# Optimization experiments

Hardware: AMD Instinct MI355X
Metric: run time of the kernel (lower is better)

The kernel has to match this reference:

```python
import jax, jax.numpy as jnp
import numpy as np

B, T, E, NH, VOCAB, MULT = 1, 1024, 768, 12, 32000, 32
N = E * MULT // NH  # 2048
LN_EPS = 1e-5


def setup_inputs() -> dict:
    key = jax.random.key(0)
    ks = jax.random.split(key, 6)
    return {
        "idx": jax.random.randint(ks[0], (B, T), 0, VOCAB),
        "embed": jax.random.normal(ks[1], (VOCAB, E), jnp.float32) * 0.02,
        "encoder": jax.random.normal(ks[2], (NH, E, N), jnp.float32) * 0.02,
        "encoder_v": jax.random.normal(ks[3], (NH, E, N), jnp.float32) * 0.02,
        "decoder": jax.random.normal(ks[4], (NH * N, E), jnp.float32) * 0.02,
        "lm_head": jax.random.normal(ks[5], (VOCAB, E), jnp.float32) * 0.02,
        "ln_w": jnp.ones((E,), jnp.float32),
        "ln_b": jnp.zeros((E,), jnp.float32),
        "n_layer": 6,
    }


def reference(idx, embed, encoder, encoder_v, decoder, lm_head, ln_w, ln_b, n_layer):
    nh, e, n = encoder.shape
    t = idx.shape[1]
    dec = decoder.reshape(nh, n, e)  # flatten order (h, n) -> h*N + n

    def ln(x):
        m = jnp.mean(x, axis=-1, keepdims=True)
        v = jnp.mean(jnp.square(x - m), axis=-1, keepdims=True)
        return (x - m) * jax.lax.rsqrt(v + LN_EPS) * ln_w + ln_b

    causal = jnp.tril(jnp.ones((t, t), bool))  # [T, T]
    scale = 1.0 / np.sqrt(n).astype(np.float32)

    x = ln(embed[idx])  # [B, T, E]  (the unsqueezed head dim broadcasts; keep it squeezed)
    for _ in range(n_layer):
        # encoder projection + ReLU: [B,T,E] x [H,E,N] -> [B,H,T,N]
        x_sparse = jax.nn.relu(jnp.einsum("bte,hen->bhtn", x, encoder))
        # hand-rolled causal attention, Q=K=x_sparse, V=x (broadcast over heads)
        scores = jnp.einsum("bhqn,bhkn->bhqk", x_sparse, x_sparse) * scale
        scores = jnp.where(causal, scores, -jnp.inf)
        attn = jax.nn.softmax(scores, axis=-1)
        y = jnp.einsum("bhqk,bke->bhqe", attn, x)  # [B,H,T,E]
        y = ln(y)
        y_sparse = jax.nn.relu(jnp.einsum("bhte,hen->bhtn", y, encoder_v))
        xy = x_sparse * y_sparse  # [B,H,T,N]; dropout p=0 -> identity
        y_mlp = jnp.einsum("bhtn,hne->bte", xy, dec)  # decoder matmul
        x = ln(x + ln(y_mlp))
    logits = jnp.einsum("bte,ve->btv", x, lm_head)
    return logits
```

## Files before the change

kernel.cpp:

```cpp
#include <hip/hip_runtime.h>

typedef unsigned short u16;
typedef short bf16x8 __attribute__((ext_vector_type(8)));
typedef float f32x4 __attribute__((ext_vector_type(4)));
typedef u16 u16x4 __attribute__((ext_vector_type(4)));

#define TT     1024
#define EE     768
#define NHH    12
#define ND     2048
#define VOC    32000
#define HNN    24576
#define NLAYER 6
#define LN_EPS 1e-5f
#define SPLITK 16

__device__ __forceinline__ float b2f(u16 u){
  unsigned int x = ((unsigned int)u) << 16; float f; __builtin_memcpy(&f, &x, 4); return f;
}
__device__ __forceinline__ u16 f2b(float f){
  unsigned int x; __builtin_memcpy(&x, &f, 4);
  x = x + 0x7fffu + ((x >> 16) & 1u);
  return (u16)(x >> 16);
}

__device__ __forceinline__ void gload16(const void* g, void* lds){
  __builtin_amdgcn_global_load_lds(
      (const __attribute__((address_space(1))) unsigned int*)g,
      (__attribute__((address_space(3))) unsigned int*)(unsigned int)(unsigned long long)lds,
      16, 0, 0);
}

__device__ __forceinline__ bf16x8 ldsr(unsigned addr){
  bf16x8 r;
  asm volatile("ds_read_b128 %0, %1" : "=v"(r) : "v"(addr));
  return r;
}

__device__ __forceinline__ void blk_sum2(float& a, float& b){
  #pragma unroll
  for (int o = 32; o > 0; o >>= 1){ a += __shfl_down(a, o); b += __shfl_down(b, o); }
  __shared__ float sa[4], sb[4];
  int lane = threadIdx.x & 63, wid = threadIdx.x >> 6;
  __syncthreads();
  if (lane == 0){ sa[wid] = a; sb[wid] = b; }
  __syncthreads();
  a = (sa[0] + sa[1]) + (sa[2] + sa[3]);
  b = (sb[0] + sb[1]) + (sb[2] + sb[3]);
}
__device__ __forceinline__ float blk_max(float v){
  #pragma unroll
  for (int o = 32; o > 0; o >>= 1) v = fmaxf(v, __shfl_down(v, o));
  __shared__ float sm[4];
  int lane = threadIdx.x & 63, wid = threadIdx.x >> 6;
  __syncthreads();
  if (lane == 0) sm[wid] = v;
  __syncthreads();
  return fmaxf(fmaxf(sm[0], sm[1]), fmaxf(sm[2], sm[3]));
}
__device__ __forceinline__ float blk_sum(float v){
  #pragma unroll
  for (int o = 32; o > 0; o >>= 1) v += __shfl_down(v, o);
  __shared__ float ss[4];
  int lane = threadIdx.x & 63, wid = threadIdx.x >> 6;
  __syncthreads();
  if (lane == 0) ss[wid] = v;
  __syncthreads();
  return (ss[0] + ss[1]) + (ss[2] + ss[3]);
}

__global__ void transpose_f2b(const float* __restrict__ in, long sIn,
                              u16* __restrict__ out, long sOut, int R, int Cc){
  __shared__ float tile[32][33];
  int z = blockIdx.z;
  in  += (long)z * sIn;
  out += (long)z * sOut;
  int c0 = blockIdx.x * 32, r0 = blockIdx.y * 32;
  int lx = threadIdx.x & 31, ly = threadIdx.x >> 5;
  #pragma unroll
  for (int i = 0; i < 32; i += 8)
    tile[ly + i][lx] = in[(long)(r0 + ly + i) * Cc + (c0 + lx)];
  __syncthreads();
  #pragma unroll
  for (int i = 0; i < 32; i += 8)
    out[(long)(c0 + ly + i) * R + (r0 + lx)] = f2b(tile[lx][ly + i]);
}

__global__ void conv_f2b(const float* __restrict__ in, u16* __restrict__ out){
  long i = ((long)blockIdx.x * 256 + threadIdx.x) * 4;
  float4 v = *(const float4*)(in + i);
  u16x4 o; o.x = f2b(v.x); o.y = f2b(v.y); o.z = f2b(v.z); o.w = f2b(v.w);
  *(u16x4*)(out + i) = o;
}

__global__ void xpose(const u16* __restrict__ in, u16* __restrict__ out){
  __shared__ u16 t[64][65];
  int e0 = blockIdx.x * 64, t0 = blockIdx.y * 64;
  int lx = threadIdx.x & 63, ly = threadIdx.x >> 6;
  #pragma unroll
  for (int i = 0; i < 64; i += 4)
    t[ly + i][lx] = in[(long)(t0 + ly + i) * EE + e0 + lx];
  __syncthreads();
  #pragma unroll
  for (int i = 0; i < 64; i += 4)
    out[(long)(e0 + ly + i) * TT + t0 + lx] = t[lx][ly + i];
}

__global__ void embed_ln(const int* __restrict__ idx, const float* __restrict__ emb,
                         const float* __restrict__ w, const float* __restrict__ b,
                         float* __restrict__ xf, u16* __restrict__ xb){
  int t = blockIdx.x, tid = threadIdx.x;
  const float* src = emb + (long)idx[t] * EE;
  float v[3];
  #pragma unroll
  for (int j = 0; j < 3; j++) v[j] = src[tid + j * 256];
  float s = v[0] + v[1] + v[2];
  float s2 = v[0]*v[0] + v[1]*v[1] + v[2]*v[2];
  blk_sum2(s, s2);
  float m  = s * (1.0f / EE);
  float var = s2 * (1.0f / EE) - m * m;
  float rs = rsqrtf(var + LN_EPS);
  #pragma unroll
  for (int j = 0; j < 3; j++){
    int e = tid + j * 256;
    float o = (v[j] - m) * rs * w[e] + b[e];
    xf[(long)t * EE + e] = o;
    xb[(long)t * EE + e] = f2b(o);
  }
}

__global__ void ln_rows(const u16* __restrict__ in, u16* __restrict__ out,
                        const float* __restrict__ w, const float* __restrict__ b){
  long row = blockIdx.x; int tid = threadIdx.x;
  const u16* src = in + row * EE;
  float v[3];
  #pragma unroll
  for (int j = 0; j < 3; j++) v[j] = b2f(src[tid + j * 256]);
  float s = v[0] + v[1] + v[2];
  float s2 = v[0]*v[0] + v[1]*v[1] + v[2]*v[2];
  blk_sum2(s, s2);
  float m = s * (1.0f / EE);
  float var = s2 * (1.0f / EE) - m * m;
  float rs = rsqrtf(var + LN_EPS);
  #pragma unroll
  for (int j = 0; j < 3; j++){
    int e = tid + j * 256;
    out[row * EE + e] = f2b((v[j] - m) * rs * w[e] + b[e]);
  }
}

__global__ void softmax_rows(const u16* __restrict__ scores, u16* __restrict__ attn){
  int q = blockIdx.x, h = blockIdx.y, tid = threadIdx.x;
  const u16* srow = scores + ((long)h * TT + q) * TT;
  u16* arow = attn + ((long)h * TT + q) * TT;
  const int len = q + 1;
  const int pad = (q + 128) & ~127;
  float v[4];
  float mx = -1e30f;
  #pragma unroll
  for (int j = 0; j < 4; j++){
    int i = tid + j * 256;
    if (i < len){ v[j] = b2f(srow[i]); mx = fmaxf(mx, v[j]); }
  }
  mx = blk_max(mx);
  float s = 0.f;
  #pragma unroll
  for (int j = 0; j < 4; j++){
    int i = tid + j * 256;
    if (i < len){ v[j] = __expf(v[j] - mx); s += v[j]; }
  }
  float inv = 1.0f / blk_sum(s);
  #pragma unroll
  for (int j = 0; j < 4; j++){
    int i = tid + j * 256;
    if (i < pad){
      u16 o = 0;
      if (i < len) o = f2b(v[j] * inv);
      arow[i] = o;
    }
  }
}

template<int P>
__global__ void residual_ln(const u16* __restrict__ part, const float* __restrict__ xin,
                            float* __restrict__ xf, u16* __restrict__ xb,
                            const float* __restrict__ w, const float* __restrict__ b){
  int t = blockIdx.x, tid = threadIdx.x;
  float g[3];
  #pragma unroll
  for (int j = 0; j < 3; j++){
    int e = tid + j * 256;
    float s = 0.f;
    #pragma unroll
    for (int pp = 0; pp < P; pp++) s += b2f(part[((long)pp * TT + t) * EE + e]);
    g[j] = s;
  }
  float s = g[0] + g[1] + g[2], s2 = g[0]*g[0] + g[1]*g[1] + g[2]*g[2];
  blk_sum2(s, s2);
  float m = s * (1.0f / EE), var = s2 * (1.0f / EE) - m * m;
  float rs = rsqrtf(var + LN_EPS);
  float hh[3];
  #pragma unroll
  for (int j = 0; j < 3; j++){
    int e = tid + j * 256;
    hh[j] = xin[(long)t * EE + e] + ((g[j] - m) * rs * w[e] + b[e]);
  }
  s = hh[0] + hh[1] + hh[2]; s2 = hh[0]*hh[0] + hh[1]*hh[1] + hh[2]*hh[2];
  blk_sum2(s, s2);
  m = s * (1.0f / EE); var = s2 * (1.0f / EE) - m * m; rs = rsqrtf(var + LN_EPS);
  #pragma unroll
  for (int j = 0; j < 3; j++){
    int e = tid + j * 256;
    float o = (hh[j] - m) * rs * w[e] + b[e];
    xf[(long)t * EE + e] = o;
    xb[(long)t * EE + e] = f2b(o);
  }
}

template<int EPI>
__global__ __launch_bounds__(512, 2)
void g8(const u16* __restrict__ Ab, long sA,
        const u16* __restrict__ Bb, long sB,
        void* __restrict__ Cb, long sC,
        int grid_m, int grid_mn,
        int K, int lda, int ldb, int ldc, float scale,
        const u16* __restrict__ Mul, long sMul, int ldmul){
  __shared__ __align__(16) u16 S[69632];

  const int nwg = gridDim.x, orig = blockIdx.x;
  const int q = nwg >> 3, r = nwg & 7, xcd = orig & 7;
  const int wgid = (xcd < r ? xcd*(q+1) : r*(q+1) + (xcd - r)*q) + (orig >> 3);
  const int z   = wgid / grid_mn;
  const int rem = wgid - z*grid_mn;
  const int nb  = rem / grid_m;
  const int mb  = rem - nb*grid_m;
  const int m0 = mb*256, n0 = nb*256;
  const int tid = threadIdx.x, lane = tid & 63, wid = tid >> 6;

  if (EPI == 2 && n0 > m0 + 255) return;

  const u16* A = Ab + (long)z*sA;
  const u16* B = Bb + (long)z*sB;

  const int rS = wid*16 + (lane >> 2);
  const int cS = (((lane & 3) ^ ((rS >> 1) & 3)) << 3);
  const u16* gA = A + (long)(m0 + rS)*lda + cS;
  const u16* gB = B + (long)(n0 + rS)*ldb + cS;

  char* Sb = (char*)&S[0];
  const unsigned db0 = 0, db1 = 65536u, scr = 131072u;
  auto issue = [&](const u16* src, unsigned dstOff){
    gload16(src, Sb + dstOff + (unsigned)wid*1024u);
  };

  const int wr = wid >> 2, wc = wid & 3;
  const int fr = lane & 15, fk = lane >> 4;
  const unsigned base = (unsigned)(unsigned long long)Sb;
  unsigned aOff[8], bOff[4];
  #pragma unroll
  for (int mi = 0; mi < 8; mi++){
    int row = wr*128 + mi*16 + fr;
    aOff[mi] = (unsigned)(row*64 + ((fk ^ ((row >> 1) & 3)) << 4));
  }
  #pragma unroll
  for (int ni = 0; ni < 4; ni++){
    int row = wc*64 + ni*16 + fr;
    bOff[ni] = 32768u + (unsigned)(row*64 + ((fk ^ ((row >> 1) & 3)) << 4));
  }

  const int NT = K >> 6;
  const long lda128 = (long)128*lda, ldb128 = (long)128*ldb;

  f32x4 acc[8][4] = {};

  issue(gA,              db0);          issue(gA + lda128,          db0 + 8192u);
  issue(gB,              db0+32768u);   issue(gB + ldb128,          db0 + 40960u);
  issue(gA + 32,         db0+16384u);   issue(gA + 32 + lda128,     db0 + 24576u);
  issue(gB + 32,         db0+49152u);   issue(gB + 32 + ldb128,     db0 + 57344u);
  issue(gA + 64,         db1);          issue(gA + 64 + lda128,     db1 + 8192u);
  issue(gB + 64,         db1+32768u);   issue(gB + 64 + ldb128,     db1 + 40960u);
  asm volatile("s_waitcnt vmcnt(8)" ::: "memory");
  __builtin_amdgcn_s_barrier();
  __builtin_amdgcn_sched_barrier(0);

  for (int t = 0; t < NT; t++){
    const unsigned cur = (t & 1) ? db1 : db0;
    const unsigned oth = (t & 1) ? db0 : db1;
    const bool v1 = (t + 1 < NT), v2 = (t + 2 < NT);
    const long k1 = (long)(v1 ? t + 1 : 0) * 64;
    const long k2 = (long)(v2 ? t + 2 : 0) * 64;
    const unsigned d1A = v1 ? oth + 16384u : scr;
    const unsigned d1B = v1 ? oth + 49152u : scr;
    const unsigned d2A = v2 ? cur           : scr;
    const unsigned d2B = v2 ? cur + 32768u  : scr;
    bf16x8 a[4], b[4];

    #pragma unroll
    for (int ni = 0; ni < 4; ni++) b[ni] = ldsr(base + cur + bOff[ni]);
    #pragma unroll
    for (int u = 0; u < 4; u++)    a[u]  = ldsr(base + cur + aOff[u]);
    issue(gA + k1 + 32, d1A); issue(gA + k1 + 32 + lda128, d1A + 8192u);
    __builtin_amdgcn_s_barrier();
    asm volatile("s_waitcnt lgkmcnt(0)" ::: "memory");
    __builtin_amdgcn_sched_barrier(0);
    __builtin_amdgcn_s_setprio(1);
    #pragma unroll
    for (int u = 0; u < 4; u++)
      #pragma unroll
      for (int ni = 0; ni < 4; ni++)
        acc[u][ni] = __builtin_amdgcn_mfma_f32_16x16x32_bf16(a[u], b[ni], acc[u][ni], 0, 0, 0);
    __builtin_amdgcn_s_setprio(0);
    __builtin_amdgcn_s_barrier();
    __builtin_amdgcn_sched_barrier(0);

    #pragma unroll
    for (int u = 0; u < 4; u++) a[u] = ldsr(base + cur + aOff[4 + u]);
    issue(gB + k1 + 32, d1B); issue(gB + k1 + 32 + ldb128, d1B + 8192u);
    __builtin_amdgcn_s_barrier();
    asm volatile("s_waitcnt lgkmcnt(0)" ::: "memory");
    __builtin_amdgcn_sched_barrier(0);
    __builtin_amdgcn_s_setprio(1);
    #pragma unroll
    for (int u = 0; u < 4; u++)
      #pragma unroll
      for (int ni = 0; ni < 4; ni++)
        acc[4+u][ni] = __builtin_amdgcn_mfma_f32_16x16x32_bf16(a[u], b[ni], acc[4+u][ni], 0, 0, 0);
    __builtin_amdgcn_s_setprio(0);
    asm volatile("s_waitcnt vmcnt(8)" ::: "memory");
    __builtin_amdgcn_s_barrier();
    __builtin_amdgcn_sched_barrier(0);

    #pragma unroll
    for (int ni = 0; ni < 4; ni++) b[ni] = ldsr(base + cur + bOff[ni] + 16384u);
    #pragma unroll
    for (int u = 0; u < 4; u++)    a[u]  = ldsr(base + cur + aOff[u] + 16384u);
    issue(gA + k2, d2A); issue(gA + k2 + lda128, d2A + 8192u);
    __builtin_amdgcn_s_barrier();
    asm volatile("s_waitcnt lgkmcnt(0)" ::: "memory");
    __builtin_amdgcn_sched_barrier(0);
    __builtin_amdgcn_s_setprio(1);
    #pragma unroll
    for (int u = 0; u < 4; u++)
      #pragma unroll
      for (int ni = 0; ni < 4; ni++)
        acc[u][ni] = __builtin_amdgcn_mfma_f32_16x16x32_bf16(a[u], b[ni], acc[u][ni], 0, 0, 0);
    __builtin_amdgcn_s_setprio(0);
    __builtin_amdgcn_s_barrier();
    __builtin_amdgcn_sched_barrier(0);

    #pragma unroll
    for (int u = 0; u < 4; u++) a[u] = ldsr(base + cur + aOff[4 + u] + 16384u);
    issue(gB + k2, d2B); issue(gB + k2 + ldb128, d2B + 8192u);
    __builtin_amdgcn_s_barrier();
    asm volatile("s_waitcnt lgkmcnt(0)" ::: "memory");
    __builtin_amdgcn_sched_barrier(0);
    __builtin_amdgcn_s_setprio(1);
    #pragma unroll
    for (int u = 0; u < 4; u++)
      #pragma unroll
      for (int ni = 0; ni < 4; ni++)
        acc[4+u][ni] = __builtin_amdgcn_mfma_f32_16x16x32_bf16(a[u], b[ni], acc[4+u][ni], 0, 0, 0);
    __builtin_amdgcn_s_setprio(0);
    asm volatile("s_waitcnt vmcnt(8)" ::: "memory");
    __builtin_amdgcn_s_barrier();
    __builtin_amdgcn_sched_barrier(0);
  }
  asm volatile("s_waitcnt vmcnt(0)" ::: "memory");

  const int er = (lane >> 4) * 4, ec = lane & 15;
  #pragma unroll
  for (int mi = 0; mi < 8; mi++){
    #pragma unroll
    for (int ni = 0; ni < 4; ni++){
      #pragma unroll
      for (int j = 0; j < 4; j++){
        int row = m0 + wr*128 + mi*16 + er + j;
        int col = n0 + wc*64 + ni*16 + ec;
        float v = acc[mi][ni][j];
        if (EPI == 0){
          ((float*)Cb + (long)z * sC)[(long)row * ldc + col] = v;
        } else if (EPI == 1){
          v = v > 0.f ? v : 0.f;
          ((u16*)Cb + (long)z * sC)[(long)row * ldc + col] = f2b(v);
        } else if (EPI == 2){
          ((u16*)Cb + (long)z * sC)[(long)row * ldc + col] = f2b(v * scale);
        } else {
          v = v > 0.f ? v : 0.f;
          float mfv = b2f((Mul + (long)z * sMul)[(long)row * ldmul + col]);
          ((u16*)Cb + (long)z * sC)[(long)row * ldc + col] = f2b(v * mfv);
        }
      }
    }
  }
}

template<int EPI, bool CCLAMP>
__global__ __launch_bounds__(256, 2)
void gemmw(const u16* __restrict__ Ab, long sA,
           const u16* __restrict__ Bb, long sB,
           void* __restrict__ Cb, long sC,
           int grid_m, int grid_mn,
           int K, int lda, int ldb, int ldc){
  constexpr unsigned BUFB = 24576u;
  __shared__ __align__(16) u16 S[3 * 12288];

  const int nwg = gridDim.x, orig = blockIdx.x;
  const int q = nwg >> 3, r = nwg & 7, xcd = orig & 7;
  const int wgid = (xcd < r ? xcd*(q+1) : r*(q+1) + (xcd - r)*q) + (orig >> 3);
  const int z   = wgid / grid_mn;
  const int rem = wgid - z*grid_mn;
  const int nb  = rem / grid_m;
  const int mb  = rem - nb*grid_m;
  const int m0 = mb*128, n0 = nb*256;
  const int tid = threadIdx.x, lane = tid & 63, wid = tid >> 6;

  const u16* A = Ab + (long)z*sA;
  const u16* B = Bb + (long)z*sB;

  const int rS = tid >> 2;
  const int cS = (((tid & 3) ^ ((rS >> 1) & 3)) << 3);
  const u16* gA[2]; const u16* gB[4];
  #pragma unroll
  for (int i = 0; i < 2; i++) gA[i] = A + (long)(m0 + i*64 + rS)*lda + cS;
  #pragma unroll
  for (int i = 0; i < 4; i++) gB[i] = B + (long)(n0 + i*64 + rS)*ldb + cS;

  char* Sb = (char*)&S[0];
  auto stage = [&](int kt, unsigned bB){
    const int ko = kt << 5;
    gload16(gA[0] + ko, Sb + bB +          wid*1024u);
    gload16(gA[1] + ko, Sb + bB +  4096u + wid*1024u);
    #pragma unroll
    for (int i = 0; i < 4; i++)
      gload16(gB[i] + ko, Sb + bB + 8192u + i*4096u + wid*1024u);
  };

  const int wr = wid >> 1, wc = wid & 1;
  const int fr = lane & 15, fk = lane >> 4;
  const unsigned base = (unsigned)(unsigned long long)Sb;
  unsigned aAd[4], bAd[8];
  #pragma unroll
  for (int mi = 0; mi < 4; mi++){
    int row = wr*64 + mi*16 + fr;
    aAd[mi] = base + (unsigned)(row*64 + ((fk ^ ((row >> 1) & 3)) << 4));
  }
  #pragma unroll
  for (int ni = 0; ni < 8; ni++){
    int row = wc*128 + ni*16 + fr;
    bAd[ni] = base + 8192u + (unsigned)(row*64 + ((fk ^ ((row >> 1) & 3)) << 4));
  }

  const int Keff = CCLAMP ? (m0 + 128 < K ? m0 + 128 : K) : K;
  const int NT = Keff >> 5;
  const int s0 = (mb*13 + nb*7 + z*5) % NT;

  f32x4 acc[4][8] = {};

  int p1 = s0 + 1; if (p1 >= NT) p1 -= NT;
  stage(s0, 0);
  stage(p1, BUFB);
  asm volatile("s_waitcnt vmcnt(6)" ::: "memory");
  __builtin_amdgcn_s_barrier();
  __builtin_amdgcn_sched_barrier(0);

  unsigned rbB = 0, wbB = 2u*BUFB;
  for (int t = 0; t < NT; t++){
    int nx = (t + 2 < NT) ? t + 2 : NT - 1;
    int ph = s0 + nx; if (ph >= NT) ph -= NT;
    stage(ph, wbB);
    bf16x8 afr[4], bfr[8];
    #pragma unroll
    for (int ni = 0; ni < 8; ni++) bfr[ni] = ldsr(bAd[ni] + rbB);
    #pragma unroll
    for (int mi = 0; mi < 4; mi++) afr[mi] = ldsr(aAd[mi] + rbB);
    __builtin_amdgcn_s_barrier();
    asm volatile("s_waitcnt lgkmcnt(0)" ::: "memory");
    __builtin_amdgcn_sched_barrier(0);
    __builtin_amdgcn_s_setprio(1);
    #pragma unroll
    for (int mi = 0; mi < 4; mi++)
      #pragma unroll
      for (int ni = 0; ni < 8; ni++)
        acc[mi][ni] = __builtin_amdgcn_mfma_f32_16x16x32_bf16(afr[mi], bfr[ni], acc[mi][ni], 0, 0, 0);
    __builtin_amdgcn_s_setprio(0);
    __builtin_amdgcn_sched_barrier(0);
    asm volatile("s_waitcnt vmcnt(6)" ::: "memory");
    __builtin_amdgcn_s_barrier();
    __builtin_amdgcn_sched_barrier(0);
    unsigned tmp = rbB; rbB += BUFB; if (rbB == 3u*BUFB) rbB = 0;
    wbB = tmp;
  }
  asm volatile("s_waitcnt vmcnt(0)" ::: "memory");

  const int er = (lane >> 4) * 4, ec = lane & 15;
  #pragma unroll
  for (int mi = 0; mi < 4; mi++){
    #pragma unroll
    for (int ni = 0; ni < 8; ni++){
      #pragma unroll
      for (int j = 0; j < 4; j++){
        int row = m0 + wr*64 + mi*16 + er + j;
        int col = n0 + wc*128 + ni*16 + ec;
        float v = acc[mi][ni][j];
        if (EPI == 0){
          ((float*)Cb + (long)z * sC)[(long)row * ldc + col] = v;
        } else {
          ((u16*)Cb + (long)z * sC)[(long)row * ldc + col] = f2b(v);
        }
      }
    }
  }
}

extern "C" void kernel_launch(void* const* d_in, const int* in_sizes, int n_in,
                              void* d_out, int out_size, void* d_ws, size_t ws_size,
                              hipStream_t stream){
  (void)in_sizes; (void)n_in; (void)out_size; (void)ws_size;
  const int*   idx     = (const int*)  d_in[0];
  const float* embed   = (const float*)d_in[1];
  const float* encoder = (const float*)d_in[2];
  const float* encv    = (const float*)d_in[3];
  const float* decoder = (const float*)d_in[4];
  const float* lm_head = (const float*)d_in[5];
  const float* ln_w    = (const float*)d_in[6];
  const float* ln_b    = (const float*)d_in[7];
  float* out = (float*)d_out;

  char* p = (char*)d_ws;
  auto take = [&](size_t n){ char* r = p; p += (n + 255) & ~(size_t)255; return r; };
  u16*   encT  = (u16*)  take((size_t)NHH * ND * EE * 2);
  u16*   encvT = (u16*)  take((size_t)NHH * ND * EE * 2);
  u16*   decT  = (u16*)  take((size_t)EE * HNN * 2);
  u16*   lmhB  = (u16*)  take((size_t)VOC * EE * 2);
  float* xf    = (float*)take((size_t)TT * EE * 4);
  u16*   xb    = (u16*)  take((size_t)TT * EE * 2);
  u16*   xT    = (u16*)  take((size_t)EE * TT * 2);
  u16*   xs    = (u16*)  take((size_t)NHH * TT * ND * 2);
  char*  big   =         take((size_t)NHH * TT * TT * 4);
  u16*   attn  = (u16*)  take((size_t)NHH * TT * TT * 2);
  u16*   yb    = (u16*)  take((size_t)NHH * TT * EE * 2);
  take((size_t)8 * TT * EE * 4);
  u16*   scores = (u16*)big;
  u16*   ybig   = (u16*)big;
  u16*   xy     = (u16*)big;
  u16*   part   = attn;

  dim3 blk(256, 1, 1);

  transpose_f2b<<<dim3(ND / 32, EE / 32, NHH), blk, 0, stream>>>(encoder, (long)EE * ND, encT,  (long)ND * EE, EE, ND);
  transpose_f2b<<<dim3(ND / 32, EE / 32, NHH), blk, 0, stream>>>(encv,    (long)EE * ND, encvT, (long)ND * EE, EE, ND);
  transpose_f2b<<<dim3(EE / 32, HNN / 32, 1),  blk, 0, stream>>>(decoder, 0, decT, 0, HNN, EE);
  conv_f2b<<<dim3((VOC * EE) / 1024, 1, 1), blk, 0, stream>>>(lm_head, lmhB);

  embed_ln<<<dim3(TT, 1, 1), blk, 0, stream>>>(idx, embed, ln_w, ln_b, xf, xb);
  xpose<<<dim3(EE / 64, TT / 64, 1), blk, 0, stream>>>(xb, xT);

  const float scl = 0.022097086912079608f;

  for (int L = 0; L < NLAYER; ++L){
    g8<1><<<dim3(4*8*NHH), dim3(512), 0, stream>>>(
        xb, 0, encT, (long)ND * EE, xs, (long)TT * ND,
        4, 32, EE, EE, EE, ND, 0.f, (const u16*)0, 0, 0);
    g8<2><<<dim3(4*4*NHH), dim3(512), 0, stream>>>(
        xs, (long)TT * ND, xs, (long)TT * ND, scores, (long)TT * TT,
        4, 16, ND, ND, ND, TT, scl, (const u16*)0, 0, 0);
    softmax_rows<<<dim3(TT, NHH, 1), blk, 0, stream>>>(scores, attn);
    gemmw<4,true><<<dim3(8*3*NHH), blk, 0, stream>>>(
        attn, (long)TT * TT, xT, 0, ybig, (long)TT * EE,
        8, 24, TT, TT, TT, EE);
    ln_rows<<<dim3(NHH * TT, 1, 1), blk, 0, stream>>>(ybig, yb, ln_w, ln_b);
    g8<3><<<dim3(4*8*NHH), dim3(512), 0, stream>>>(
        yb, (long)TT * EE, encvT, (long)ND * EE, xy, (long)ND,
        4, 32, EE, EE, EE, HNN, 0.f, xs, (long)TT * ND, ND);
    gemmw<4,false><<<dim3(8*3*SPLITK), blk, 0, stream>>>(
        xy, (long)(HNN / SPLITK), decT, (long)(HNN / SPLITK), part, (long)TT * EE,
        8, 24, HNN / SPLITK, HNN, HNN, EE);
    residual_ln<SPLITK><<<dim3(TT, 1, 1), blk, 0, stream>>>(part, xf, xf, xb, ln_w, ln_b);
    xpose<<<dim3(EE / 64, TT / 64, 1), blk, 0, stream>>>(xb, xT);
  }

  g8<0><<<dim3(4*125), dim3(512), 0, stream>>>(
      xb, 0, lmhB, 0, out, 0,
      4, 500, EE, EE, EE, VOC, 0.f, (const u16*)0, 0, 0);
}
```

Before: 1.927 ms.

## Fuse weight prep kernels, vectorize row kernels, rotate GEMM K start

Merges the four weight transpose and convert launches into one prep kernel. The layernorm, softmax and residual row kernels move to 4-wide vector loads and stores with 192 active threads. The g8 GEMM now starts its K loop at a per-tile rotated offset and wraps around, which removes the scratch LDS region for out-of-range prefetches and shrinks shared memory. The rotation is meant to spread concurrent tiles across different K slices of memory, at the cost of a changed summation order.

```diff
diff --git a/kernel.cpp b/kernel.cpp
--- a/kernel.cpp
+++ b/kernel.cpp
@@ -69,28 +69,44 @@
   return (ss[0] + ss[1]) + (ss[2] + ss[3]);
 }
 
-__global__ void transpose_f2b(const float* __restrict__ in, long sIn,
-                              u16* __restrict__ out, long sOut, int R, int Cc){
+__global__ void prep(const float* __restrict__ enc, const float* __restrict__ encv,
+                     const float* __restrict__ dec, const float* __restrict__ lmh,
+                     u16* __restrict__ encT, u16* __restrict__ encvT,
+                     u16* __restrict__ decT, u16* __restrict__ lmhB){
   __shared__ float tile[32][33];
-  int z = blockIdx.z;
-  in  += (long)z * sIn;
-  out += (long)z * sOut;
-  int c0 = blockIdx.x * 32, r0 = blockIdx.y * 32;
+  int b = blockIdx.x;
   int lx = threadIdx.x & 31, ly = threadIdx.x >> 5;
-  #pragma unroll
-  for (int i = 0; i < 32; i += 8)
-    tile[ly + i][lx] = in[(long)(r0 + ly + i) * Cc + (c0 + lx)];
-  __syncthreads();
-  #pragma unroll
-  for (int i = 0; i < 32; i += 8)
-    out[(long)(c0 + ly + i) * R + (r0 + lx)] = f2b(tile[lx][ly + i]);
-}
-
-__global__ void conv_f2b(const float* __restrict__ in, u16* __restrict__ out){
-  long i = ((long)blockIdx.x * 256 + threadIdx.x) * 4;
-  float4 v = *(const float4*)(in + i);
-  u16x4 o; o.x = f2b(v.x); o.y = f2b(v.y); o.z = f2b(v.z); o.w = f2b(v.w);
-  *(u16x4*)(out + i) = o;
+  if (b < 36864){
+    const float* in; u16* out;
+    if (b < 18432){ in = enc; out = encT; } else { in = encv; out = encvT; b -= 18432; }
+    int z = b / 1536, rem = b - z * 1536;
+    int c0 = (rem & 63) * 32, r0 = (rem >> 6) * 32;
+    in  += (long)z * EE * ND;
+    out += (long)z * ND * EE;
+    #pragma unroll
+    for (int i = 0; i < 32; i += 8)
+      tile[ly + i][lx] = in[(long)(r0 + ly + i) * ND + c0 + lx];
+    __syncthreads();
+    #pragma unroll
+    for (int i = 0; i < 32; i += 8)
+      out[(long)(c0 + ly + i) * EE + r0 + lx] = f2b(tile[lx][ly + i]);
+  } else if (b < 55296){
+    b -= 36864;
+    int c0 = (b % 24) * 32, r0 = (b / 24) * 32;
+    #pragma unroll
+    for (int i = 0; i < 32; i += 8)
+      tile[ly + i][lx] = dec[(long)(r0 + ly + i) * EE + c0 + lx];
+    __syncthreads();
+    #pragma unroll
+    for (int i = 0; i < 32; i += 8)
+      decT[(long)(c0 + ly + i) * HNN + r0 + lx] = f2b(tile[lx][ly + i]);
+  } else {
+    b -= 55296;
+    long i = ((long)b * 256 + threadIdx.x) * 4;
+    float4 v = *(const float4*)(lmh + i);
+    u16x4 o; o.x = f2b(v.x); o.y = f2b(v.y); o.z = f2b(v.z); o.w = f2b(v.w);
+    *(u16x4*)(lmhB + i) = o;
+  }
 }
 
 __global__ void xpose(const u16* __restrict__ in, u16* __restrict__ out){
@@ -111,21 +127,28 @@
                          float* __restrict__ xf, u16* __restrict__ xb){
   int t = blockIdx.x, tid = threadIdx.x;
   const float* src = emb + (long)idx[t] * EE;
-  float v[3];
-  #pragma unroll
-  for (int j = 0; j < 3; j++) v[j] = src[tid + j * 256];
-  float s = v[0] + v[1] + v[2];
-  float s2 = v[0]*v[0] + v[1]*v[1] + v[2]*v[2];
+  float v[4] = {0.f, 0.f, 0.f, 0.f};
+  if (tid < 192){
+    float4 r = *(const float4*)&src[tid * 4];
+    v[0] = r.x; v[1] = r.y; v[2] = r.z; v[3] = r.w;
+  }
+  float s = (v[0] + v[1]) + (v[2] + v[3]);
+  float s2 = (v[0]*v[0] + v[1]*v[1]) + (v[2]*v[2] + v[3]*v[3]);
   blk_sum2(s, s2);
   float m  = s * (1.0f / EE);
   float var = s2 * (1.0f / EE) - m * m;
   float rs = rsqrtf(var + LN_EPS);
-  #pragma unroll
-  for (int j = 0; j < 3; j++){
-    int e = tid + j * 256;
-    float o = (v[j] - m) * rs * w[e] + b[e];
-    xf[(long)t * EE + e] = o;
-    xb[(long)t * EE + e] = f2b(o);
+  if (tid < 192){
+    int e0 = tid * 4;
+    float4 o; u16x4 ob;
+    float* op = &o.x;
+    #pragma unroll
+    for (int j = 0; j < 4; j++){
+      float ov = (v[j] - m) * rs * w[e0 + j] + b[e0 + j];
+      op[j] = ov; ob[j] = f2b(ov);
+    }
+    *(float4*)&xf[(long)t * EE + e0] = o;
+    *(u16x4*)&xb[(long)t * EE + e0] = ob;
   }
 }
 
@@ -133,19 +156,24 @@
                         const float* __restrict__ w, const float* __restrict__ b){
   long row = blockIdx.x; int tid = threadIdx.x;
   const u16* src = in + row * EE;
-  float v[3];
-  #pragma unroll
-  for (int j = 0; j < 3; j++) v[j] = b2f(src[tid + j * 256]);
-  float s = v[0] + v[1] + v[2];
-  float s2 = v[0]*v[0] + v[1]*v[1] + v[2]*v[2];
+  float v[4] = {0.f, 0.f, 0.f, 0.f};
+  if (tid < 192){
+    u16x4 r = *(const u16x4*)&src[tid * 4];
+    #pragma unroll
+    for (int j = 0; j < 4; j++) v[j] = b2f(r[j]);
+  }
+  float s = (v[0] + v[1]) + (v[2] + v[3]);
+  float s2 = (v[0]*v[0] + v[1]*v[1]) + (v[2]*v[2] + v[3]*v[3]);
   blk_sum2(s, s2);
   float m = s * (1.0f / EE);
   float var = s2 * (1.0f / EE) - m * m;
   float rs = rsqrtf(var + LN_EPS);
-  #pragma unroll
-  for (int j = 0; j < 3; j++){
-    int e = tid + j * 256;
-    out[row * EE + e] = f2b((v[j] - m) * rs * w[e] + b[e]);
+  if (tid < 192){
+    int e0 = tid * 4;
+    u16x4 ob;
+    #pragma unroll
+    for (int j = 0; j < 4; j++) ob[j] = f2b((v[j] - m) * rs * w[e0 + j] + b[e0 + j]);
+    *(u16x4*)&out[row * EE + e0] = ob;
   }
 }
 
@@ -155,29 +183,30 @@
   u16* arow = attn + ((long)h * TT + q) * TT;
   const int len = q + 1;
   const int pad = (q + 128) & ~127;
+  u16x4 raw = *(const u16x4*)&srow[tid * 4];
   float v[4];
   float mx = -1e30f;
   #pragma unroll
   for (int j = 0; j < 4; j++){
-    int i = tid + j * 256;
-    if (i < len){ v[j] = b2f(srow[i]); mx = fmaxf(mx, v[j]); }
+    int i = tid * 4 + j;
+    v[j] = (i < len) ? b2f(raw[j]) : -1e30f;
+    mx = fmaxf(mx, v[j]);
   }
   mx = blk_max(mx);
   float s = 0.f;
   #pragma unroll
   for (int j = 0; j < 4; j++){
-    int i = tid + j * 256;
-    if (i < len){ v[j] = __expf(v[j] - mx); s += v[j]; }
+    int i = tid * 4 + j;
+    float e = (i < len) ? __expf(v[j] - mx) : 0.f;
+    v[j] = e; s += e;
   }
   float inv = 1.0f / blk_sum(s);
-  #pragma unroll
-  for (int j = 0; j < 4; j++){
-    int i = tid + j * 256;
-    if (i < pad){
-      u16 o = 0;
-      if (i < len) o = f2b(v[j] * inv);
-      arow[i] = o;
-    }
+  int i0 = tid * 4;
+  if (i0 < pad){
+    u16x4 o;
+    #pragma unroll
+    for (int j = 0; j < 4; j++) o[j] = (i0 + j < len) ? f2b(v[j] * inv) : (u16)0;
+    *(u16x4*)&arow[i0] = o;
   }
 }
 
@@ -186,34 +215,45 @@
                             float* __restrict__ xf, u16* __restrict__ xb,
                             const float* __restrict__ w, const float* __restrict__ b){
   int t = blockIdx.x, tid = threadIdx.x;
-  float g[3];
-  #pragma unroll
-  for (int j = 0; j < 3; j++){
-    int e = tid + j * 256;
-    float s = 0.f;
-    #pragma unroll
-    for (int pp = 0; pp < P; pp++) s += b2f(part[((long)pp * TT + t) * EE + e]);
-    g[j] = s;
-  }
-  float s = g[0] + g[1] + g[2], s2 = g[0]*g[0] + g[1]*g[1] + g[2]*g[2];
+  float g[4] = {0.f, 0.f, 0.f, 0.f};
+  if (tid < 192){
+    int e0 = tid * 4;
+    #pragma unroll
+    for (int pp = 0; pp < P; pp++){
+      u16x4 r = *(const u16x4*)&part[((long)pp * TT + t) * EE + e0];
+      #pragma unroll
+      for (int j = 0; j < 4; j++) g[j] += b2f(r[j]);
+    }
+  }
+  float s = (g[0] + g[1]) + (g[2] + g[3]);
+  float s2 = (g[0]*g[0] + g[1]*g[1]) + (g[2]*g[2] + g[3]*g[3]);
   blk_sum2(s, s2);
   float m = s * (1.0f / EE), var = s2 * (1.0f / EE) - m * m;
   float rs = rsqrtf(var + LN_EPS);
-  float hh[3];
-  #pragma unroll
-  for (int j = 0; j < 3; j++){
-    int e = tid + j * 256;
-    hh[j] = xin[(long)t * EE + e] + ((g[j] - m) * rs * w[e] + b[e]);
-  }
-  s = hh[0] + hh[1] + hh[2]; s2 = hh[0]*hh[0] + hh[1]*hh[1] + hh[2]*hh[2];
+  float hh[4] = {0.f, 0.f, 0.f, 0.f};
+  if (tid < 192){
+    int e0 = tid * 4;
+    float4 xi = *(const float4*)&xin[(long)t * EE + e0];
+    const float* xp = &xi.x;
+    #pragma unroll
+    for (int j = 0; j < 4; j++)
+      hh[j] = xp[j] + ((g[j] - m) * rs * w[e0 + j] + b[e0 + j]);
+  }
+  s = (hh[0] + hh[1]) + (hh[2] + hh[3]);
+  s2 = (hh[0]*hh[0] + hh[1]*hh[1]) + (hh[2]*hh[2] + hh[3]*hh[3]);
   blk_sum2(s, s2);
   m = s * (1.0f / EE); var = s2 * (1.0f / EE) - m * m; rs = rsqrtf(var + LN_EPS);
-  #pragma unroll
-  for (int j = 0; j < 3; j++){
-    int e = tid + j * 256;
-    float o = (hh[j] - m) * rs * w[e] + b[e];
-    xf[(long)t * EE + e] = o;
-    xb[(long)t * EE + e] = f2b(o);
+  if (tid < 192){
+    int e0 = tid * 4;
+    float4 o; u16x4 ob;
+    float* op = &o.x;
+    #pragma unroll
+    for (int j = 0; j < 4; j++){
+      float ov = (hh[j] - m) * rs * w[e0 + j] + b[e0 + j];
+      op[j] = ov; ob[j] = f2b(ov);
+    }
+    *(float4*)&xf[(long)t * EE + e0] = o;
+    *(u16x4*)&xb[(long)t * EE + e0] = ob;
   }
 }
 
@@ -225,7 +265,7 @@
         int grid_m, int grid_mn,
         int K, int lda, int ldb, int ldc, float scale,
         const u16* __restrict__ Mul, long sMul, int ldmul){
-  __shared__ __align__(16) u16 S[69632];
+  __shared__ __align__(16) u16 S[65536];
 
   const int nwg = gridDim.x, orig = blockIdx.x;
   const int q = nwg >> 3, r = nwg & 7, xcd = orig & 7;
@@ -248,7 +288,7 @@
   const u16* gB = B + (long)(n0 + rS)*ldb + cS;
 
   char* Sb = (char*)&S[0];
-  const unsigned db0 = 0, db1 = 65536u, scr = 131072u;
+  const unsigned db0 = 0, db1 = 65536u;
   auto issue = [&](const u16* src, unsigned dstOff){
     gload16(src, Sb + dstOff + (unsigned)wid*1024u);
   };
@@ -269,30 +309,33 @@
   }
 
   const int NT = K >> 6;
+  const int s0 = ((mb*3 + nb*5 + z)*7) % NT;
   const long lda128 = (long)128*lda, ldb128 = (long)128*ldb;
 
   f32x4 acc[8][4] = {};
 
-  issue(gA,              db0);          issue(gA + lda128,          db0 + 8192u);
-  issue(gB,              db0+32768u);   issue(gB + ldb128,          db0 + 40960u);
-  issue(gA + 32,         db0+16384u);   issue(gA + 32 + lda128,     db0 + 24576u);
-  issue(gB + 32,         db0+49152u);   issue(gB + 32 + ldb128,     db0 + 57344u);
-  issue(gA + 64,         db1);          issue(gA + 64 + lda128,     db1 + 8192u);
-  issue(gB + 64,         db1+32768u);   issue(gB + 64 + ldb128,     db1 + 40960u);
+  int p1 = s0 + 1; if (p1 >= NT) p1 -= NT;
+  {
+    const long kp0 = (long)s0*64, kp1 = (long)p1*64;
+    issue(gA + kp0,            db0);          issue(gA + kp0 + lda128,      db0 + 8192u);
+    issue(gB + kp0,            db0+32768u);   issue(gB + kp0 + ldb128,      db0 + 40960u);
+    issue(gA + kp0 + 32,       db0+16384u);   issue(gA + kp0 + 32 + lda128, db0 + 24576u);
+    issue(gB + kp0 + 32,       db0+49152u);   issue(gB + kp0 + 32 + ldb128, db0 + 57344u);
+    issue(gA + kp1,            db1);          issue(gA + kp1 + lda128,      db1 + 8192u);
+    issue(gB + kp1,            db1+32768u);   issue(gB + kp1 + ldb128,      db1 + 40960u);
+  }
   asm volatile("s_waitcnt vmcnt(8)" ::: "memory");
   __builtin_amdgcn_s_barrier();
   __builtin_amdgcn_sched_barrier(0);
 
+  int t1 = p1;
+  int t2 = p1 + 1; if (t2 >= NT) t2 -= NT;
   for (int t = 0; t < NT; t++){
     const unsigned cur = (t & 1) ? db1 : db0;
     const unsigned oth = (t & 1) ? db0 : db1;
-    const bool v1 = (t + 1 < NT), v2 = (t + 2 < NT);
-    const long k1 = (long)(v1 ? t + 1 : 0) * 64;
-    const long k2 = (long)(v2 ? t + 2 : 0) * 64;
-    const unsigned d1A = v1 ? oth + 16384u : scr;
-    const unsigned d1B = v1 ? oth + 49152u : scr;
-    const unsigned d2A = v2 ? cur           : scr;
-    const unsigned d2B = v2 ? cur + 32768u  : scr;
+    const long k1 = (long)t1*64, k2 = (long)t2*64;
+    const unsigned d1A = oth + 16384u, d1B = oth + 49152u;
+    const unsigned d2A = cur,          d2B = cur + 32768u;
     bf16x8 a[4], b[4];
 
     #pragma unroll
@@ -364,6 +407,9 @@
     asm volatile("s_waitcnt vmcnt(8)" ::: "memory");
     __builtin_amdgcn_s_barrier();
     __builtin_amdgcn_sched_barrier(0);
+
+    t1 = t2;
+    t2 = t2 + 1; if (t2 >= NT) t2 -= NT;
   }
   asm volatile("s_waitcnt vmcnt(0)" ::: "memory");
 
@@ -547,10 +593,8 @@
 
   dim3 blk(256, 1, 1);
 
-  transpose_f2b<<<dim3(ND / 32, EE / 32, NHH), blk, 0, stream>>>(encoder, (long)EE * ND, encT,  (long)ND * EE, EE, ND);
-  transpose_f2b<<<dim3(ND / 32, EE / 32, NHH), blk, 0, stream>>>(encv,    (long)EE * ND, encvT, (long)ND * EE, EE, ND);
-  transpose_f2b<<<dim3(EE / 32, HNN / 32, 1),  blk, 0, stream>>>(decoder, 0, decT, 0, HNN, EE);
-  conv_f2b<<<dim3((VOC * EE) / 1024, 1, 1), blk, 0, stream>>>(lm_head, lmhB);
+  prep<<<dim3(79296, 1, 1), blk, 0, stream>>>(encoder, encv, decoder, lm_head,
+                                              encT, encvT, decT, lmhB);
 
   embed_ln<<<dim3(TT, 1, 1), blk, 0, stream>>>(idx, embed, ln_w, ln_b, xf, xb);
   xpose<<<dim3(EE / 64, TT / 64, 1), blk, 0, stream>>>(xb, xT);
```

After: 1.949 ms. No clear change (+1.1%).
